# Optimization experiments

Hardware: AMD Instinct MI355X
Metric: run time of the kernel (lower is better)

The kernel has to match this reference:

```python
import jax, jax.numpy as jnp
import numpy as np

B, N, D_MODEL, H, D_K, D_V = 2, 2048, 1024, 16, 64, 64


def setup_inputs() -> dict:
    key = jax.random.key(0)
    ks = jax.random.split(key, 8)
    queries = jax.random.normal(ks[0], (B, N, D_MODEL), dtype=jnp.float32)
    keys = jax.random.normal(ks[1], (B, N, D_MODEL), dtype=jnp.float32)
    values = jax.random.normal(ks[2], (B, N, D_MODEL), dtype=jnp.float32)
    # nn.Linear weights: (out_features, in_features); init.normal_(std=0.001) in the
    # original, but we use a larger scale for a numerically meaningful test.
    Wq = jax.random.normal(ks[3], (H * D_K, D_MODEL), dtype=jnp.float32) * 0.02
    Wk = jax.random.normal(ks[4], (H * D_K, D_MODEL), dtype=jnp.float32) * 0.02
    Wv = jax.random.normal(ks[5], (H * D_V, D_MODEL), dtype=jnp.float32) * 0.02
    Wo = jax.random.normal(ks[6], (D_MODEL, H * D_V), dtype=jnp.float32) * 0.02
    bo = jnp.zeros((D_MODEL,), dtype=jnp.float32)
    return {"queries": queries, "keys": keys, "values": values,
            "Wq": Wq, "Wk": Wk, "Wv": Wv, "Wo": Wo, "bo": bo}


def reference(queries, keys, values, Wq, Wk, Wv, Wo, bo):
    b, nq, _ = queries.shape
    nk = keys.shape[1]
    scale = 1.0 / np.sqrt(D_K).astype(np.float32)
    # projections: (b, n, h, d)
    q = (queries @ Wq.T).reshape(b, nq, H, D_K)
    k = (keys @ Wk.T).reshape(b, nk, H, D_K)
    v = (values @ Wv.T).reshape(b, nk, H, D_V)
    # scaled dot-product attention; seq_mask=None, attention_weights=None, dropout p=0
    att = jnp.einsum('bqhd,bkhd->bhqk', q, k) * scale  # (b, h, nq, nk)
    att = jax.nn.softmax(att, axis=-1)
    out = jnp.einsum('bhqk,bkhd->bqhd', att, v).reshape(b, nq, H * D_V)
    return queries + (out @ Wo.T + bo)
```

## Files before the change

kernel.cpp:

```cpp
#include <hip/hip_runtime.h>
#include <hip/hip_bf16.h>
#include <stdint.h>

#define BATCH  2
#define SEQ    2048
#define DMODEL 1024
#define NHEAD  16
#define DHEAD  64

typedef unsigned short u16;
typedef __attribute__((ext_vector_type(8))) short bf16x8;
typedef __attribute__((ext_vector_type(4))) float f32x4;

__device__ __forceinline__ u16 f2bf(float x) {
    union { float f; uint32_t u; } v; v.f = x;
    uint32_t r = v.u + 0x7fffu + ((v.u >> 16) & 1u);
    return (u16)(r >> 16);
}

__device__ __forceinline__ uint32_t pk2bf(float a, float b) {
    __hip_bfloat162 h = __float22bfloat162_rn(make_float2(a, b));
    return *(uint32_t*)&h;
}

__device__ __forceinline__ float exp2_raw(float x) {
    float r;
    asm("v_exp_f32 %0, %1" : "=v"(r) : "v"(x));
    return r;
}

__device__ __forceinline__ void gload_lds16(const void* g, void* l) {
    __builtin_amdgcn_global_load_lds(
        (const __attribute__((address_space(1))) uint32_t*)(uintptr_t)g,
        (__attribute__((address_space(3))) uint32_t*)(uintptr_t)l,
        16, 0, 0);
}

__device__ __forceinline__ f32x4 mfma16(bf16x8 a, bf16x8 b, f32x4 c) {
    return __builtin_amdgcn_mfma_f32_16x16x32_bf16(a, b, c, 0, 0, 0);
}

__global__ __launch_bounds__(256) void cvt7_kernel(
    const float* s0, const float* s1, const float* s2, const float* s3,
    const float* s4, const float* s5, const float* s6,
    u16* d0, u16* d1, u16* d2, u16* d3, u16* d4, u16* d5, u16* d6)
{
    const float* s; u16* d; size_t n;
    switch (blockIdx.y) {
        case 0: s = s0; d = d0; n = (size_t)BATCH * SEQ * DMODEL; break;
        case 1: s = s1; d = d1; n = (size_t)BATCH * SEQ * DMODEL; break;
        case 2: s = s2; d = d2; n = (size_t)BATCH * SEQ * DMODEL; break;
        case 3: s = s3; d = d3; n = (size_t)DMODEL * DMODEL; break;
        case 4: s = s4; d = d4; n = (size_t)DMODEL * DMODEL; break;
        case 5: s = s5; d = d5; n = (size_t)DMODEL * DMODEL; break;
        default: s = s6; d = d6; n = (size_t)DMODEL * DMODEL; break;
    }
    size_t i = ((size_t)blockIdx.x * 256 + threadIdx.x) * 8;
    if (i >= n) return;
    float4 a = *(const float4*)(s + i);
    float4 b = *(const float4*)(s + i + 4);
    union { uint4 v; u16 e[8]; } u;
    u.e[0] = f2bf(a.x); u.e[1] = f2bf(a.y); u.e[2] = f2bf(a.z); u.e[3] = f2bf(a.w);
    u.e[4] = f2bf(b.x); u.e[5] = f2bf(b.y); u.e[6] = f2bf(b.z); u.e[7] = f2bf(b.w);
    *(uint4*)(d + i) = u.v;
}

__device__ __forceinline__ void gemm_core_128(
    const u16* __restrict__ A, const u16* __restrict__ Bm, int K,
    int brow, int bcol, u16* As, u16* Bs, f32x4 (&acc)[4][4])
{
    const int tid  = threadIdx.x;
    const int lane = tid & 63;
    const int wr   = ((tid >> 6) >> 1) * 64;
    const int wc   = ((tid >> 6) & 1) * 64;
    const int srow = tid >> 2;
    const int scol = (tid & 3) * 8;
    const int fr   = lane & 15;
    const int fk   = (lane >> 4) * 8;

    for (int k0 = 0; k0 < K; k0 += 32) {
        gload_lds16(A  + (size_t)(brow + srow) * K + k0 + scol,       As + srow * 32 + scol);
        gload_lds16(A  + (size_t)(brow + 64 + srow) * K + k0 + scol,  As + (64 + srow) * 32 + scol);
        gload_lds16(Bm + (size_t)(bcol + srow) * K + k0 + scol,       Bs + srow * 32 + scol);
        gload_lds16(Bm + (size_t)(bcol + 64 + srow) * K + k0 + scol,  Bs + (64 + srow) * 32 + scol);
        __syncthreads();
        bf16x8 af[4], bfv[4];
        #pragma unroll
        for (int i = 0; i < 4; ++i) {
            af[i]  = *(const bf16x8*)(As + (wr + i * 16 + fr) * 32 + fk);
            bfv[i] = *(const bf16x8*)(Bs + (wc + i * 16 + fr) * 32 + fk);
        }
        #pragma unroll
        for (int am = 0; am < 4; ++am)
            #pragma unroll
            for (int bn = 0; bn < 4; ++bn)
                acc[am][bn] = mfma16(af[am], bfv[bn], acc[am][bn]);
        __syncthreads();
    }
}

__device__ __forceinline__ void gemm_core_64x128(
    const u16* __restrict__ A, const u16* __restrict__ Bm, int K,
    int brow, int bcol, u16* As, u16* Bs, f32x4 (&acc)[4][2])
{
    const int tid  = threadIdx.x;
    const int lane = tid & 63;
    const int wc   = (tid >> 6) * 32;
    const int srow = tid >> 2;
    const int scol = (tid & 3) * 8;
    const int fr   = lane & 15;
    const int fk   = (lane >> 4) * 8;

    for (int k0 = 0; k0 < K; k0 += 32) {
        gload_lds16(A  + (size_t)(brow + srow) * K + k0 + scol,       As + srow * 32 + scol);
        gload_lds16(Bm + (size_t)(bcol + srow) * K + k0 + scol,       Bs + srow * 32 + scol);
        gload_lds16(Bm + (size_t)(bcol + 64 + srow) * K + k0 + scol,  Bs + (64 + srow) * 32 + scol);
        __syncthreads();
        bf16x8 af[4], bfv[2];
        #pragma unroll
        for (int i = 0; i < 4; ++i)
            af[i]  = *(const bf16x8*)(As + (i * 16 + fr) * 32 + fk);
        #pragma unroll
        for (int i = 0; i < 2; ++i)
            bfv[i] = *(const bf16x8*)(Bs + (wc + i * 16 + fr) * 32 + fk);
        #pragma unroll
        for (int am = 0; am < 4; ++am)
            #pragma unroll
            for (int bn = 0; bn < 2; ++bn)
                acc[am][bn] = mfma16(af[am], bfv[bn], acc[am][bn]);
        __syncthreads();
    }
}

__global__ __launch_bounds__(256) void gemm_qkv_kernel(
    const u16* __restrict__ Xq, const u16* __restrict__ Xk, const u16* __restrict__ Xv,
    const u16* __restrict__ Wq, const u16* __restrict__ Wk, const u16* __restrict__ Wv,
    u16* __restrict__ Qo, u16* __restrict__ Ko, u16* __restrict__ Vo,
    int M, int Nn, int K)
{
    __shared__ u16 As[128 * 32];
    __shared__ u16 Bs[128 * 32];
    const int z = blockIdx.z;
    const u16* A  = (z == 0) ? Xq : (z == 1) ? Xk : Xv;
    const u16* Bm = (z == 0) ? Wq : (z == 1) ? Wk : Wv;
    u16* D        = (z == 0) ? Qo : (z == 1) ? Ko : Vo;
    const float scale = (z == 0) ? 0.18033688011112042f : 1.0f;

    const int lin  = blockIdx.y * gridDim.x + blockIdx.x;
    const int nlin = (lin & 7) * 32 + (lin >> 3);
    const int brow = (nlin >> 3) * 128;
    const int bcol = (nlin & 7) * 128;
    f32x4 acc[4][4];
    #pragma unroll
    for (int am = 0; am < 4; ++am)
        #pragma unroll
        for (int bn = 0; bn < 4; ++bn)
            acc[am][bn] = (f32x4){0.f, 0.f, 0.f, 0.f};

    gemm_core_128(A, Bm, K, brow, bcol, As, Bs, acc);

    const int lane = threadIdx.x & 63;
    const int wr = ((threadIdx.x >> 6) >> 1) * 64;
    const int wc = ((threadIdx.x >> 6) & 1) * 64;
    const int fr = lane & 15;
    const int fj4 = (lane >> 4) * 4;
    #pragma unroll
    for (int am = 0; am < 4; ++am)
        #pragma unroll
        for (int bn = 0; bn < 4; ++bn)
            #pragma unroll
            for (int j = 0; j < 4; ++j) {
                int row = brow + wr + am * 16 + fj4 + j;
                int col = bcol + wc + bn * 16 + fr;
                D[(size_t)row * Nn + col] = f2bf(acc[am][bn][j] * scale);
            }
}

__global__ __launch_bounds__(256, 2) void gemm_out_kernel(
    const u16* __restrict__ A, const u16* __restrict__ Bm,
    const float* __restrict__ bias, const float* __restrict__ resid,
    float* __restrict__ D, int M, int Nn, int K)
{
    __shared__ u16 As[64 * 32];
    __shared__ u16 Bs[128 * 32];

    const int lin  = blockIdx.y * gridDim.x + blockIdx.x;
    const int nlin = (lin & 7) * 64 + (lin >> 3);
    const int brow = (nlin >> 3) * 64;
    const int bcol = (nlin & 7) * 128;
    f32x4 acc[4][2];
    #pragma unroll
    for (int am = 0; am < 4; ++am)
        #pragma unroll
        for (int bn = 0; bn < 2; ++bn)
            acc[am][bn] = (f32x4){0.f, 0.f, 0.f, 0.f};

    gemm_core_64x128(A, Bm, K, brow, bcol, As, Bs, acc);

    const int lane = threadIdx.x & 63;
    const int wc = (threadIdx.x >> 6) * 32;
    const int fr = lane & 15;
    const int fj4 = (lane >> 4) * 4;
    #pragma unroll
    for (int am = 0; am < 4; ++am)
        #pragma unroll
        for (int bn = 0; bn < 2; ++bn)
            #pragma unroll
            for (int j = 0; j < 4; ++j) {
                int row = brow + am * 16 + fj4 + j;
                int col = bcol + wc + bn * 16 + fr;
                D[(size_t)row * Nn + col] = acc[am][bn][j] + bias[col] + resid[(size_t)row * Nn + col];
            }
}

__global__ __launch_bounds__(256) void vtrans_kernel(
    const u16* __restrict__ V, u16* __restrict__ Vt)
{
    __shared__ u16 T[64][66];
    const int tid = threadIdx.x;
    const int bh  = blockIdx.y;
    const int kv0 = blockIdx.x * 64;
    const size_t rowbase = (size_t)(bh >> 4) * SEQ;
    const int colbase = (bh & 15) * DHEAD;

    {
        const int r = tid >> 2;
        const int c = (tid & 3) * 16;
        const u16* src = V + (rowbase + kv0 + r) * DMODEL + colbase + c;
        uint4 a = *(const uint4*)(src);
        uint4 b = *(const uint4*)(src + 8);
        uint32_t* dst = (uint32_t*)&T[r][c];
        dst[0] = a.x; dst[1] = a.y; dst[2] = a.z; dst[3] = a.w;
        dst[4] = b.x; dst[5] = b.y; dst[6] = b.z; dst[7] = b.w;
    }
    __syncthreads();
    {
        const int d = tid >> 2;
        const int c = (tid & 3) * 16;
        union { uint4 v; u16 e[8]; } o0, o1;
        #pragma unroll
        for (int j = 0; j < 8; ++j) o0.e[j] = T[c + j][d];
        #pragma unroll
        for (int j = 0; j < 8; ++j) o1.e[j] = T[c + 8 + j][d];
        u16* dst = Vt + (size_t)bh * DHEAD * SEQ + (size_t)d * SEQ + kv0 + c;
        *(uint4*)(dst) = o0.v;
        *(uint4*)(dst + 8) = o1.v;
    }
}

__global__ __launch_bounds__(1024, 1) void attn_kernel(
    const u16* __restrict__ Qb, const u16* __restrict__ Kb, const u16* __restrict__ Vt,
    u16* __restrict__ AO)
{
    __shared__ u16 Ks[3][64 * 64];
    __shared__ u16 Vs[3][64 * 64];
    __shared__ u16 Ps[256 * 72];

    const int tid  = threadIdx.x;
    const int lane = tid & 63;
    const int wave = tid >> 6;

    const int lin  = blockIdx.x;
    const int nlin = (lin & 7) * 32 + (lin >> 3);
    const int qblk = nlin & 7;
    const int bh   = nlin >> 3;

    const size_t rowbase = (size_t)(bh >> 4) * SEQ;
    const int colbase = (bh & 15) * DHEAD;
    const int q0 = qblk * 256;
    const int fr  = lane & 15;
    const int g   = lane >> 4;
    const int fk  = g * 8;
    const int fj4 = g * 4;
    const int qw  = wave * 16;

    const u16* Kh = Kb + rowbase * DMODEL + colbase;
    const u16* Vh = Vt + (size_t)bh * DHEAD * SEQ;

    const int st  = tid & 511;
    const int sr  = st >> 3;
    const int sc  = st & 7;
    const int scs = (sc ^ (sr & 7)) << 3;
    const int sdst = sr * 64 + sc * 8;
    const bool stageK = (tid < 512);

    bf16x8 qf[2];
    #pragma unroll
    for (int kc = 0; kc < 2; ++kc)
        qf[kc] = *(const bf16x8*)(Qb + (rowbase + q0 + qw + fr) * DMODEL
                                     + colbase + kc * 32 + fk);

    f32x4 oacc[4];
    float lsum = 0.f;
    #pragma unroll
    for (int dn = 0; dn < 4; ++dn) oacc[dn] = (f32x4){0.f, 0.f, 0.f, 0.f};

    if (stageK) {
        gload_lds16(Kh + (size_t)sr * DMODEL + scs,        &Ks[0][sdst]);
        gload_lds16(Kh + (size_t)(64 + sr) * DMODEL + scs, &Ks[1][sdst]);
    } else {
        gload_lds16(Vh + (size_t)sr * SEQ + scs,           &Vs[0][sdst]);
        gload_lds16(Vh + (size_t)sr * SEQ + 64 + scs,      &Vs[1][sdst]);
    }

    const int NT = SEQ / 64;
    int cur = 0;
    for (int t = 0; t < NT; ++t) {
        if (t < NT - 1) {
            asm volatile("s_waitcnt vmcnt(1)" ::: "memory");
        } else {
            asm volatile("s_waitcnt vmcnt(0)" ::: "memory");
        }
        __builtin_amdgcn_s_barrier();
        __builtin_amdgcn_sched_barrier(0);

        if (t + 2 < NT) {
            int wbuf = cur + 2; if (wbuf >= 3) wbuf -= 3;
            const size_t kvn = (size_t)(t + 2) * 64;
            if (stageK) gload_lds16(Kh + (kvn + sr) * DMODEL + scs,    &Ks[wbuf][sdst]);
            else        gload_lds16(Vh + (size_t)sr * SEQ + kvn + scs, &Vs[wbuf][sdst]);
        }

        const u16* K0 = &Ks[cur][0];
        const u16* V0 = &Vs[cur][0];

        f32x4 sacc[4];
        #pragma unroll
        for (int bn = 0; bn < 4; ++bn) sacc[bn] = (f32x4){0.f, 0.f, 0.f, 0.f};
        __builtin_amdgcn_s_setprio(1);
        #pragma unroll
        for (int bn = 0; bn < 4; ++bn) {
            bf16x8 kf0 = *(const bf16x8*)(K0 + (bn * 16 + fr) * 64 + (((g)     ^ (fr & 7)) << 3));
            bf16x8 kf1 = *(const bf16x8*)(K0 + (bn * 16 + fr) * 64 + (((4 + g) ^ (fr & 7)) << 3));
            sacc[bn] = mfma16(kf0, qf[0], sacc[bn]);
            sacc[bn] = mfma16(kf1, qf[1], sacc[bn]);
        }
        __builtin_amdgcn_s_setprio(0);

        {
            float lacc = 0.f;
            #pragma unroll
            for (int bn = 0; bn < 4; ++bn) {
                float p0 = exp2_raw(sacc[bn][0]);
                float p1 = exp2_raw(sacc[bn][1]);
                float p2 = exp2_raw(sacc[bn][2]);
                float p3 = exp2_raw(sacc[bn][3]);
                uint2 w;
                w.x = pk2bf(p0, p1);
                w.y = pk2bf(p2, p3);
                *(uint2*)(Ps + (qw + fr) * 72 + bn * 16 + fj4) = w;
                lacc += (p0 + p1) + (p2 + p3);
            }
            lsum += lacc;
        }

        bf16x8 pf[2];
        #pragma unroll
        for (int kc = 0; kc < 2; ++kc)
            pf[kc] = *(const bf16x8*)(Ps + (qw + fr) * 72 + kc * 32 + fk);
        __builtin_amdgcn_s_setprio(1);
        #pragma unroll
        for (int dn = 0; dn < 4; ++dn) {
            bf16x8 vf0 = *(const bf16x8*)(V0 + (dn * 16 + fr) * 64 + (((g)     ^ (fr & 7)) << 3));
            bf16x8 vf1 = *(const bf16x8*)(V0 + (dn * 16 + fr) * 64 + (((4 + g) ^ (fr & 7)) << 3));
            oacc[dn] = mfma16(pf[0], vf0, oacc[dn]);
            oacc[dn] = mfma16(pf[1], vf1, oacc[dn]);
        }
        __builtin_amdgcn_s_setprio(0);

        cur = (cur == 2) ? 0 : cur + 1;
    }

    float invj[4];
    {
        float l = lsum;
        l += __shfl_xor(l, 16);
        l += __shfl_xor(l, 32);
        #pragma unroll
        for (int j = 0; j < 4; ++j) {
            float lj = __shfl(l, (lane & 48) | (fj4 + j));
            invj[j] = 1.f / lj;
        }
    }

    #pragma unroll
    for (int dn = 0; dn < 4; ++dn)
        #pragma unroll
        for (int j = 0; j < 4; ++j) {
            int row = q0 + qw + fj4 + j;
            AO[(rowbase + row) * DMODEL + colbase + dn * 16 + fr] =
                f2bf(oacc[dn][j] * invj[j]);
        }
}

extern "C" void kernel_launch(void* const* d_in, const int* in_sizes, int n_in,
                              void* d_out, int out_size, void* d_ws, size_t ws_size,
                              hipStream_t stream)
{
    const float* q_f  = (const float*)d_in[0];
    const float* k_f  = (const float*)d_in[1];
    const float* v_f  = (const float*)d_in[2];
    const float* Wq_f = (const float*)d_in[3];
    const float* Wk_f = (const float*)d_in[4];
    const float* Wv_f = (const float*)d_in[5];
    const float* Wo_f = (const float*)d_in[6];
    const float* bo_f = (const float*)d_in[7];

    char* ws = (char*)d_ws;
    const size_t ACT = (size_t)BATCH * SEQ * DMODEL * sizeof(u16);
    const size_t WSZ = (size_t)DMODEL * DMODEL * sizeof(u16);
    u16* Xq  = (u16*)(ws);
    u16* Xk  = (u16*)(ws + ACT);
    u16* Xv  = (u16*)(ws + 2 * ACT);
    u16* Wqb = (u16*)(ws + 3 * ACT);
    u16* Wkb = (u16*)(ws + 3 * ACT + WSZ);
    u16* Wvb = (u16*)(ws + 3 * ACT + 2 * WSZ);
    u16* Wob = (u16*)(ws + 3 * ACT + 3 * WSZ);
    u16* Qb  = (u16*)(ws + 3 * ACT + 4 * WSZ);
    u16* Kb  = (u16*)(ws + 4 * ACT + 4 * WSZ);
    u16* Vb  = (u16*)(ws + 5 * ACT + 4 * WSZ);
    u16* AO  = (u16*)(ws + 6 * ACT + 4 * WSZ);
    u16* Vt  = Xq;

    const int M = BATCH * SEQ;
    const int Nn = DMODEL;
    const int K = DMODEL;

    cvt7_kernel<<<dim3(2048, 7, 1), 256, 0, stream>>>(
        q_f, k_f, v_f, Wq_f, Wk_f, Wv_f, Wo_f,
        Xq, Xk, Xv, Wqb, Wkb, Wvb, Wob);

    gemm_qkv_kernel<<<dim3(Nn / 128, M / 128, 3), 256, 0, stream>>>(
        Xq, Xk, Xv, Wqb, Wkb, Wvb, Qb, Kb, Vb, M, Nn, K);

    vtrans_kernel<<<dim3(SEQ / 64, BATCH * NHEAD, 1), 256, 0, stream>>>(Vb, Vt);

    attn_kernel<<<dim3(256, 1, 1), 1024, 0, stream>>>(Qb, Kb, Vt, AO);

    gemm_out_kernel<<<dim3(Nn / 128, M / 64, 1), 256, 0, stream>>>(
        AO, Wob, bo_f, q_f, (float*)d_out, M, Nn, K);
}
```

Measured before the change: 125.6 us.

## Widen KV tiles to 128 and compute softmax row sums via MFMA with ones

Doubles the per-iteration KV tile from 64 to 128 rows, with all threads staging both K and V each step, which halves the number of loop iterations and block-wide barriers. Each tile is processed in two 64-column halves that reuse the P scratch buffer. The softmax denominator is now accumulated by an extra MFMA of the bf16 P fragments against a ones vector instead of scalar adds plus final shuffles. The change doubles LDS use for K/V buffers, and the row sums now come from bf16-rounded probabilities, matching what the PV product uses.

```diff
diff --git a/kernel.cpp b/kernel.cpp
--- a/kernel.cpp
+++ b/kernel.cpp
@@ -252,8 +252,8 @@
     const u16* __restrict__ Qb, const u16* __restrict__ Kb, const u16* __restrict__ Vt,
     u16* __restrict__ AO)
 {
-    __shared__ u16 Ks[3][64 * 64];
-    __shared__ u16 Vs[3][64 * 64];
+    __shared__ u16 Ks[3][128 * 64];
+    __shared__ u16 Vs[3][64 * 128];
     __shared__ u16 Ps[256 * 72];
 
     const int tid  = threadIdx.x;
@@ -277,12 +277,14 @@
     const u16* Kh = Kb + rowbase * DMODEL + colbase;
     const u16* Vh = Vt + (size_t)bh * DHEAD * SEQ;
 
-    const int st  = tid & 511;
-    const int sr  = st >> 3;
-    const int sc  = st & 7;
-    const int scs = (sc ^ (sr & 7)) << 3;
-    const int sdst = sr * 64 + sc * 8;
-    const bool stageK = (tid < 512);
+    const int kr   = tid >> 3;
+    const int kc8  = tid & 7;
+    const int kscs = (kc8 ^ (kr & 7)) << 3;
+    const int kdst = kr * 64 + kc8 * 8;
+    const int vd   = tid >> 4;
+    const int vc   = tid & 15;
+    const int vcs  = (((vc & 7) ^ (vd & 7)) | (vc & 8)) << 3;
+    const int vdst = vd * 128 + vc * 8;
 
     bf16x8 qf[2];
     #pragma unroll
@@ -290,24 +292,25 @@
         qf[kc] = *(const bf16x8*)(Qb + (rowbase + q0 + qw + fr) * DMODEL
                                      + colbase + kc * 32 + fk);
 
+    bf16x8 onesb;
+    #pragma unroll
+    for (int i = 0; i < 8; ++i) onesb[i] = (short)0x3F80;
+
     f32x4 oacc[4];
-    float lsum = 0.f;
+    f32x4 lacc = (f32x4){0.f, 0.f, 0.f, 0.f};
     #pragma unroll
     for (int dn = 0; dn < 4; ++dn) oacc[dn] = (f32x4){0.f, 0.f, 0.f, 0.f};
 
-    if (stageK) {
-        gload_lds16(Kh + (size_t)sr * DMODEL + scs,        &Ks[0][sdst]);
-        gload_lds16(Kh + (size_t)(64 + sr) * DMODEL + scs, &Ks[1][sdst]);
-    } else {
-        gload_lds16(Vh + (size_t)sr * SEQ + scs,           &Vs[0][sdst]);
-        gload_lds16(Vh + (size_t)sr * SEQ + 64 + scs,      &Vs[1][sdst]);
-    }
-
-    const int NT = SEQ / 64;
+    gload_lds16(Kh + (size_t)kr * DMODEL + kscs,          &Ks[0][kdst]);
+    gload_lds16(Vh + (size_t)vd * SEQ + vcs,              &Vs[0][vdst]);
+    gload_lds16(Kh + (size_t)(128 + kr) * DMODEL + kscs,  &Ks[1][kdst]);
+    gload_lds16(Vh + (size_t)vd * SEQ + 128 + vcs,        &Vs[1][vdst]);
+
+    const int NT = SEQ / 128;
     int cur = 0;
     for (int t = 0; t < NT; ++t) {
         if (t < NT - 1) {
-            asm volatile("s_waitcnt vmcnt(1)" ::: "memory");
+            asm volatile("s_waitcnt vmcnt(2)" ::: "memory");
         } else {
             asm volatile("s_waitcnt vmcnt(0)" ::: "memory");
         }
@@ -316,29 +319,29 @@
 
         if (t + 2 < NT) {
             int wbuf = cur + 2; if (wbuf >= 3) wbuf -= 3;
-            const size_t kvn = (size_t)(t + 2) * 64;
-            if (stageK) gload_lds16(Kh + (kvn + sr) * DMODEL + scs,    &Ks[wbuf][sdst]);
-            else        gload_lds16(Vh + (size_t)sr * SEQ + kvn + scs, &Vs[wbuf][sdst]);
+            const size_t kvn = (size_t)(t + 2) * 128;
+            gload_lds16(Kh + (kvn + kr) * DMODEL + kscs,   &Ks[wbuf][kdst]);
+            gload_lds16(Vh + (size_t)vd * SEQ + kvn + vcs, &Vs[wbuf][vdst]);
         }
 
         const u16* K0 = &Ks[cur][0];
         const u16* V0 = &Vs[cur][0];
 
-        f32x4 sacc[4];
-        #pragma unroll
-        for (int bn = 0; bn < 4; ++bn) sacc[bn] = (f32x4){0.f, 0.f, 0.f, 0.f};
-        __builtin_amdgcn_s_setprio(1);
-        #pragma unroll
-        for (int bn = 0; bn < 4; ++bn) {
-            bf16x8 kf0 = *(const bf16x8*)(K0 + (bn * 16 + fr) * 64 + (((g)     ^ (fr & 7)) << 3));
-            bf16x8 kf1 = *(const bf16x8*)(K0 + (bn * 16 + fr) * 64 + (((4 + g) ^ (fr & 7)) << 3));
-            sacc[bn] = mfma16(kf0, qf[0], sacc[bn]);
-            sacc[bn] = mfma16(kf1, qf[1], sacc[bn]);
-        }
-        __builtin_amdgcn_s_setprio(0);
-
-        {
-            float lacc = 0.f;
+        #pragma unroll
+        for (int h = 0; h < 2; ++h) {
+            f32x4 sacc[4];
+            #pragma unroll
+            for (int bn = 0; bn < 4; ++bn) sacc[bn] = (f32x4){0.f, 0.f, 0.f, 0.f};
+            __builtin_amdgcn_s_setprio(1);
+            #pragma unroll
+            for (int bn = 0; bn < 4; ++bn) {
+                bf16x8 kf0 = *(const bf16x8*)(K0 + (h * 64 + bn * 16 + fr) * 64 + (((g)     ^ (fr & 7)) << 3));
+                bf16x8 kf1 = *(const bf16x8*)(K0 + (h * 64 + bn * 16 + fr) * 64 + (((4 + g) ^ (fr & 7)) << 3));
+                sacc[bn] = mfma16(kf0, qf[0], sacc[bn]);
+                sacc[bn] = mfma16(kf1, qf[1], sacc[bn]);
+            }
+            __builtin_amdgcn_s_setprio(0);
+
             #pragma unroll
             for (int bn = 0; bn < 4; ++bn) {
                 float p0 = exp2_raw(sacc[bn][0]);
@@ -349,39 +352,31 @@
                 w.x = pk2bf(p0, p1);
                 w.y = pk2bf(p2, p3);
                 *(uint2*)(Ps + (qw + fr) * 72 + bn * 16 + fj4) = w;
-                lacc += (p0 + p1) + (p2 + p3);
             }
-            lsum += lacc;
+
+            bf16x8 pf[2];
+            #pragma unroll
+            for (int kc = 0; kc < 2; ++kc)
+                pf[kc] = *(const bf16x8*)(Ps + (qw + fr) * 72 + kc * 32 + fk);
+            __builtin_amdgcn_s_setprio(1);
+            #pragma unroll
+            for (int dn = 0; dn < 4; ++dn) {
+                bf16x8 vf0 = *(const bf16x8*)(V0 + (dn * 16 + fr) * 128 + ((h * 8 + ((g)     ^ (fr & 7))) << 3));
+                bf16x8 vf1 = *(const bf16x8*)(V0 + (dn * 16 + fr) * 128 + ((h * 8 + ((4 + g) ^ (fr & 7))) << 3));
+                oacc[dn] = mfma16(pf[0], vf0, oacc[dn]);
+                oacc[dn] = mfma16(pf[1], vf1, oacc[dn]);
+            }
+            lacc = mfma16(pf[0], onesb, lacc);
+            lacc = mfma16(pf[1], onesb, lacc);
+            __builtin_amdgcn_s_setprio(0);
         }
 
-        bf16x8 pf[2];
-        #pragma unroll
-        for (int kc = 0; kc < 2; ++kc)
-            pf[kc] = *(const bf16x8*)(Ps + (qw + fr) * 72 + kc * 32 + fk);
-        __builtin_amdgcn_s_setprio(1);
-        #pragma unroll
-        for (int dn = 0; dn < 4; ++dn) {
-            bf16x8 vf0 = *(const bf16x8*)(V0 + (dn * 16 + fr) * 64 + (((g)     ^ (fr & 7)) << 3));
-            bf16x8 vf1 = *(const bf16x8*)(V0 + (dn * 16 + fr) * 64 + (((4 + g) ^ (fr & 7)) << 3));
-            oacc[dn] = mfma16(pf[0], vf0, oacc[dn]);
-            oacc[dn] = mfma16(pf[1], vf1, oacc[dn]);
-        }
-        __builtin_amdgcn_s_setprio(0);
-
         cur = (cur == 2) ? 0 : cur + 1;
     }
 
     float invj[4];
-    {
-        float l = lsum;
-        l += __shfl_xor(l, 16);
-        l += __shfl_xor(l, 32);
-        #pragma unroll
-        for (int j = 0; j < 4; ++j) {
-            float lj = __shfl(l, (lane & 48) | (fj4 + j));
-            invj[j] = 1.f / lj;
-        }
-    }
+    #pragma unroll
+    for (int j = 0; j < 4; ++j) invj[j] = 1.f / lacc[j];
 
     #pragma unroll
     for (int dn = 0; dn < 4; ++dn)
```

Result: no change. 125.7 us (+0.1%).
